# Performance work log

Hardware: AMD Instinct MI355X
Metric: run time of the kernel (lower is better)

The kernel has to match this reference:

```python
import jax, jax.numpy as jnp
import numpy as np
from jax import lax

B = 16384
D_MODEL = 84
N_EXPERTS = 2
TOP_K = 2
HIDDEN = 2048


def _conv(x, w, b):
    # x: [N,C,H,W], w: [O,I,kh,kw] (torch OIHW), VALID padding, stride 1
    y = lax.conv_general_dilated(x, w, (1, 1), 'VALID',
                                 dimension_numbers=('NCHW', 'OIHW', 'NCHW'))
    return y + b[None, :, None, None]


def _maxpool2(x):
    return lax.reduce_window(x, -jnp.inf, lax.max,
                             (1, 1, 2, 2), (1, 1, 2, 2), 'VALID')


def setup_inputs() -> dict:
    key = jax.random.key(0)
    ks = jax.random.split(key, 17)
    s = 0.05
    return {
        'x': jax.random.normal(ks[0], (B, 3, 32, 32), jnp.float32),
        'conv1_w': jax.random.normal(ks[1], (6, 3, 5, 5), jnp.float32) * s,
        'conv1_b': jax.random.normal(ks[2], (6,), jnp.float32) * s,
        'conv2_w': jax.random.normal(ks[3], (16, 6, 5, 5), jnp.float32) * s,
        'conv2_b': jax.random.normal(ks[4], (16,), jnp.float32) * s,
        'fc1_w': jax.random.normal(ks[5], (400, 120), jnp.float32) * s,
        'fc1_b': jax.random.normal(ks[6], (120,), jnp.float32) * s,
        'fc2_w': jax.random.normal(ks[7], (120, 84), jnp.float32) * s,
        'fc2_b': jax.random.normal(ks[8], (84,), jnp.float32) * s,
        'gate_w': jax.random.normal(ks[9], (D_MODEL, N_EXPERTS), jnp.float32) * s,
        'exp_w1': jax.random.normal(ks[10], (N_EXPERTS, D_MODEL, HIDDEN), jnp.float32) * s,
        'exp_b1': jax.random.normal(ks[11], (N_EXPERTS, HIDDEN), jnp.float32) * s,
        'exp_w2': jax.random.normal(ks[12], (N_EXPERTS, HIDDEN, D_MODEL), jnp.float32) * s,
        'exp_b2': jax.random.normal(ks[13], (N_EXPERTS, D_MODEL), jnp.float32) * s,
        'fc3_w': jax.random.normal(ks[14], (84, 10), jnp.float32) * s,
        'fc3_b': jax.random.normal(ks[15], (10,), jnp.float32) * s,
    }


def _moe(x, gate_w, exp_w1, exp_b1, exp_w2, exp_b2):
    # tutel top-k gate: softmax over expert logits, select top-k, renormalize
    n = x.shape[0]
    scores = jax.nn.softmax(x @ gate_w, axis=-1)          # [N,E]
    top_v, top_i = lax.top_k(scores, TOP_K)               # [N,k]
    gates = top_v / jnp.sum(top_v, axis=-1, keepdims=True)
    # dense combine weights [N,E] (zero where not routed)
    comb = jnp.zeros((n, N_EXPERTS), x.dtype).at[
        jnp.arange(n)[:, None], top_i].set(gates)
    # grouped expert FFN (E=2: evaluate both, weight-combine)
    h = jax.nn.relu(jnp.einsum('nd,edh->enh', x, exp_w1) + exp_b1[:, None, :])
    y = jnp.einsum('enh,ehd->end', h, exp_w2) + exp_b2[:, None, :]  # [E,N,D]
    return jnp.einsum('ne,end->nd', comb, y)


def reference(x, conv1_w, conv1_b, conv2_w, conv2_b, fc1_w, fc1_b,
              fc2_w, fc2_b, gate_w, exp_w1, exp_b1, exp_w2, exp_b2,
              fc3_w, fc3_b):
    h = _maxpool2(jax.nn.relu(_conv(x, conv1_w, conv1_b)))   # [B,6,14,14]
    h = _maxpool2(jax.nn.relu(_conv(h, conv2_w, conv2_b)))   # [B,16,5,5]
    h = h.reshape(-1, 16 * 5 * 5)                            # [B,400]
    h = jax.nn.relu(h @ fc1_w + fc1_b)                       # [B,120]
    h = jax.nn.relu(h @ fc2_w + fc2_b)                       # [B,84]
    h = _moe(h, gate_w, exp_w1, exp_b1, exp_w2, exp_b2)      # [B,84]
    return h @ fc3_w + fc3_b                                 # [B,10]
```

## Files before the change

### kernel.cpp

```cpp
#include <hip/hip_runtime.h>
#include <stdint.h>

typedef unsigned short u16;
typedef __attribute__((ext_vector_type(8))) short s8v;
typedef __attribute__((ext_vector_type(4))) float f4v;
typedef __fp16 h2v __attribute__((ext_vector_type(2)));

__device__ __forceinline__ float bu2f(u16 u) {
  return __uint_as_float(((uint32_t)u) << 16);
}
__device__ __forceinline__ u16 f2bu(float f) {
  uint32_t u = __float_as_uint(f);
  u += 0x7fffu + ((u >> 16) & 1u);
  return (u16)(u >> 16);
}
__device__ __forceinline__ u16 f2h16(float f) {
  __fp16 h = (__fp16)f;
  u16 r;
  __builtin_memcpy(&r, &h, 2);
  return r;
}
__device__ __forceinline__ float ldin(int m, const void* p, long i) {
  return m ? ((const float*)p)[i] : bu2f(((const u16*)p)[i]);
}

union U32H2 { uint32_t u; h2v h; };

__device__ __forceinline__ uint32_t pk2h(float a, float b) {
  U32H2 x;
  x.h = __builtin_amdgcn_cvt_pkrtz(a, b);
  return x.u;
}

#if __has_builtin(__builtin_amdgcn_fdot2)
__device__ __forceinline__ float fdot2u(uint32_t a, uint32_t b, float c) {
  U32H2 ua, ub;
  ua.u = a; ub.u = b;
  return __builtin_amdgcn_fdot2(ua.h, ub.h, c, false);
}
#else
__device__ __forceinline__ float fdot2u(uint32_t a, uint32_t b, float c) {
  U32H2 ua, ub;
  ua.u = a; ub.u = b;
  c = fmaf((float)ua.h.x, (float)ub.h.x, c);
  return fmaf((float)ua.h.y, (float)ub.h.y, c);
}
#endif

__global__ __launch_bounds__(256) void k_init(
    const u16* __restrict__ x,
    const void* __restrict__ c1w, const void* __restrict__ c1b,
    const void* __restrict__ c2w, const void* __restrict__ c2b,
    int* __restrict__ flag, uint32_t* __restrict__ cdw) {
  __shared__ int s[256];
  __shared__ int smode;
  const int tid = threadIdx.x;
  int cnt = 0;
  for (int i = tid; i < 2048; i += 256) {
    int e = (x[i] >> 7) & 0xFF;
    cnt += (e >= 96 && e <= 134) ? 1 : 0;
  }
  s[tid] = cnt;
  __syncthreads();
  if (tid == 0) {
    int t = 0;
    for (int i = 0; i < 256; ++i) t += s[i];
    int m = (t >= 1843) ? 0 : 1;
    *flag = m;
    smode = m;
  }
  __syncthreads();
  const int mode = smode;
  for (int i = tid; i < 1732; i += 256) {
    if (i < 270) {
      int p = i % 3, ky = (i / 3) % 5, ic = (i / 15) % 3, c = i / 45;
      long b = (((long)c * 3 + ic) * 5 + ky) * 5;
      float w0 = ldin(mode, c1w, b + 2 * p);
      float w1 = (2 * p + 1 < 5) ? ldin(mode, c1w, b + 2 * p + 1) : 0.f;
      cdw[i] = (uint32_t)f2h16(w0) | ((uint32_t)f2h16(w1) << 16);
    } else if (i < 1710) {
      int j = i - 270;
      int p = j % 3, ky = (j / 3) % 5, ic = (j / 15) % 6, c = j / 90;
      long b = (((long)c * 6 + ic) * 5 + ky) * 5;
      float w0 = ldin(mode, c2w, b + 2 * p);
      float w1 = (2 * p + 1 < 5) ? ldin(mode, c2w, b + 2 * p + 1) : 0.f;
      cdw[i] = (uint32_t)f2h16(w0) | ((uint32_t)f2h16(w1) << 16);
    } else if (i < 1716) {
      ((float*)(cdw + 1710))[i - 1710] = ldin(mode, c1b, i - 1710);
    } else {
      ((float*)(cdw + 1716))[i - 1716] = ldin(mode, c2b, i - 1716);
    }
  }
}

#define CIMG 5
#define SXW 38
__global__ __launch_bounds__(256, 3) void k_conv(
    const int* __restrict__ flag,
    const void* __restrict__ x,
    const uint32_t* __restrict__ cdw,
    const void* __restrict__ fc1w, const void* __restrict__ fc2w,
    const void* __restrict__ ew1, const void* __restrict__ ew2,
    u16* __restrict__ p2,
    u16* __restrict__ fc1t, u16* __restrict__ fc2t,
    u16* __restrict__ w1t, u16* __restrict__ w2t,
    int Btot) {
  __shared__ u16 sxh[CIMG * 3 * 32 * SXW];
  __shared__ u16 sp1h[CIMG * 6 * 14 * 18];
  const int mode = *flag;
  const uint32_t* cd1 = cdw;
  const uint32_t* cd2 = cdw + 270;
  const float* cb1 = (const float*)(cdw + 1710);
  const float* cb2 = (const float*)(cdw + 1716);
  const int tid = threadIdx.x;
  const long gimg0 = (long)blockIdx.x * CIMG;

  for (int r = tid; r < CIMG * 96; r += 256) {
    *(uint32_t*)(sxh + (size_t)r * SXW + 32) = 0;
    *(uint32_t*)(sxh + (size_t)r * SXW + 34) = 0;
    *(uint32_t*)(sxh + (size_t)r * SXW + 36) = 0;
  }
  for (int r = tid; r < CIMG * 84; r += 256) {
    *(uint32_t*)(sp1h + (size_t)r * 18 + 14) = 0;
    *(uint32_t*)(sp1h + (size_t)r * 18 + 16) = 0;
  }

  for (int i = tid; i < CIMG * 96; i += 256) {
    int img = i / 96, rem = i - img * 96;
    if (gimg0 + img < Btot) {
      long goff = (gimg0 + img) * 3072 + (long)rem * 32;
      u16* dst = sxh + (size_t)i * SXW;
      if (!mode) {
        const uint32_t* src = (const uint32_t*)((const u16*)x + goff);
#pragma unroll
        for (int j = 0; j < 16; ++j) {
          uint32_t d = src[j];
          *(uint32_t*)(dst + 2 * j) =
              pk2h(__uint_as_float(d << 16), __uint_as_float(d & 0xffff0000u));
        }
      } else {
        const float* src = (const float*)x + goff;
#pragma unroll
        for (int j = 0; j < 16; ++j)
          *(uint32_t*)(dst + 2 * j) = pk2h(src[2 * j], src[2 * j + 1]);
      }
    }
  }
  __syncthreads();

  for (int task = tid; task < CIMG * 196; task += 256) {
    int img = task / 196, pos = task - img * 196;
    if (gimg0 + img >= Btot) continue;
    int py = pos / 14, px = pos - py * 14;
    int x0 = 2 * px, y0 = 2 * py;
    float acc[6][4];
#pragma unroll
    for (int c = 0; c < 6; ++c) {
      float bv = cb1[c];
      acc[c][0] = bv; acc[c][1] = bv; acc[c][2] = bv; acc[c][3] = bv;
    }
    for (int ic = 0; ic < 3; ++ic) {
      uint32_t A[6][4], S[6][3];
      const u16* rb = sxh + ((size_t)(img * 3 + ic) * 32 + y0) * SXW + x0;
#pragma unroll
      for (int r = 0; r < 6; ++r) {
#pragma unroll
        for (int p = 0; p < 4; ++p)
          A[r][p] = *(const uint32_t*)(rb + (size_t)r * SXW + 2 * p);
#pragma unroll
        for (int p = 0; p < 3; ++p)
          S[r][p] = (A[r][p] >> 16) | (A[r][p + 1] << 16);
      }
#pragma unroll
      for (int c = 0; c < 6; ++c) {
        const uint32_t* wb = cd1 + ((c * 3 + ic) * 5) * 3;
#pragma unroll
        for (int ky = 0; ky < 5; ++ky) {
#pragma unroll
          for (int p = 0; p < 3; ++p) {
            uint32_t w = wb[ky * 3 + p];
            acc[c][0] = fdot2u(A[ky][p], w, acc[c][0]);
            acc[c][1] = fdot2u(S[ky][p], w, acc[c][1]);
            acc[c][2] = fdot2u(A[ky + 1][p], w, acc[c][2]);
            acc[c][3] = fdot2u(S[ky + 1][p], w, acc[c][3]);
          }
        }
      }
    }
#pragma unroll
    for (int c = 0; c < 6; ++c) {
      float m = fmaxf(0.f, fmaxf(fmaxf(acc[c][0], acc[c][1]),
                                 fmaxf(acc[c][2], acc[c][3])));
      sp1h[((size_t)(img * 6 + c) * 14 + py) * 18 + px] = f2h16(m);
    }
  }
  __syncthreads();

  for (int task = tid; task < CIMG * 100; task += 256) {
    int img = task / 100, r0 = task - img * 100;
    if (gimg0 + img >= Btot) continue;
    int grp = r0 / 25, pos = r0 - grp * 25;
    int py = pos / 5, px = pos - py * 5;
    int x0 = 2 * px, y0 = 2 * py;
    int c0 = grp * 4;
    float acc[4][4];
#pragma unroll
    for (int c = 0; c < 4; ++c) {
      float bv = cb2[c0 + c];
      acc[c][0] = bv; acc[c][1] = bv; acc[c][2] = bv; acc[c][3] = bv;
    }
    for (int ic = 0; ic < 6; ++ic) {
      uint32_t A[6][4], S[6][3];
      const u16* rb = sp1h + ((size_t)(img * 6 + ic) * 14 + y0) * 18 + x0;
#pragma unroll
      for (int r = 0; r < 6; ++r) {
#pragma unroll
        for (int p = 0; p < 4; ++p)
          A[r][p] = *(const uint32_t*)(rb + (size_t)r * 18 + 2 * p);
#pragma unroll
        for (int p = 0; p < 3; ++p)
          S[r][p] = (A[r][p] >> 16) | (A[r][p + 1] << 16);
      }
#pragma unroll
      for (int c = 0; c < 4; ++c) {
        const uint32_t* wb = cd2 + (((c0 + c) * 6 + ic) * 5) * 3;
#pragma unroll
        for (int ky = 0; ky < 5; ++ky) {
#pragma unroll
          for (int p = 0; p < 3; ++p) {
            uint32_t w = wb[ky * 3 + p];
            acc[c][0] = fdot2u(A[ky][p], w, acc[c][0]);
            acc[c][1] = fdot2u(S[ky][p], w, acc[c][1]);
            acc[c][2] = fdot2u(A[ky + 1][p], w, acc[c][2]);
            acc[c][3] = fdot2u(S[ky + 1][p], w, acc[c][3]);
          }
        }
      }
    }
    u16* pout = p2 + (gimg0 + img) * 416;
#pragma unroll
    for (int c = 0; c < 4; ++c) {
      float m = fmaxf(0.f, fmaxf(fmaxf(acc[c][0], acc[c][1]),
                                 fmaxf(acc[c][2], acc[c][3])));
      pout[(c0 + c) * 25 + py * 5 + px] = f2bu(m);
    }
  }

  for (int i = tid; i < CIMG * 16; i += 256) {
    int img = i / 16;
    if (gimg0 + img < Btot) p2[(gimg0 + img) * 416 + 400 + (i & 15)] = 0;
  }

  {
    long base = (long)blockIdx.x * 260;
    long end = base + 260;
    if (end > 851968) end = 851968;
    for (long gid = base + tid; gid < end; gid += 256) {
      if (gid < 53248) {
        int n = (int)(gid / 416), k = (int)(gid % 416);
        fc1t[gid] = (n < 120 && k < 400)
                        ? f2bu(ldin(mode, fc1w, (long)k * 120 + n)) : (u16)0;
      } else if (gid < 65536) {
        long i = gid - 53248;
        int n = (int)(i / 128), k = (int)(i % 128);
        fc2t[i] = (n < 84 && k < 120)
                      ? f2bu(ldin(mode, fc2w, (long)k * 84 + n)) : (u16)0;
      } else if (gid < 458752) {
        long i = gid - 65536;
        int e = (int)(i / 196608);
        long r = i % 196608;
        int n = (int)(r / 96), k = (int)(r % 96);
        w1t[i] = (k < 84)
                     ? f2bu(ldin(mode, ew1, ((long)e * 84 + k) * 2048 + n)) : (u16)0;
      } else {
        long i = gid - 458752;
        int e = (int)(i / 196608);
        long r = i % 196608;
        int n = (int)(r / 2048), k = (int)(r % 2048);
        w2t[i] = (n < 84)
                     ? f2bu(ldin(mode, ew2, ((long)e * 2048 + k) * 84 + n)) : (u16)0;
      }
    }
  }
}

__global__ __launch_bounds__(256, 2) void k_fcA(
    const int* __restrict__ flag,
    const u16* __restrict__ p2,
    const u16* __restrict__ fc1t, const u16* __restrict__ fc2t,
    const void* __restrict__ fc1b, const void* __restrict__ fc2b,
    const void* __restrict__ gw,
    u16* __restrict__ a2buf, float* __restrict__ scbuf) {
  __shared__ __align__(16) char smem[62976];
  u16* a2s = (u16*)smem;
  u16* hs = (u16*)(smem + 13312);
  u16* wbuf = (u16*)(smem + 31232);
  u16* xs = (u16*)(smem + 57856);

  const int mode = *flag;
  const int tid = threadIdx.x;
  const int wv = tid >> 6, ln = tid & 63;
  const int m = ln & 15, quad = ln >> 4;
  const long t0 = (long)blockIdx.x * 64;
  const int row0 = wv * 16 + quad * 4;

  for (int i = tid; i < 30720 / 4; i += 256) ((uint32_t*)smem)[i] = 0;

  f4v acc1[8];
#pragma unroll
  for (int i = 0; i < 8; ++i) acc1[i] = (f4v){0.f, 0.f, 0.f, 0.f};
  for (int s = 0; s < 13; ++s) {
    {
      int r = tid >> 2, c0 = (tid & 3) * 8;
      *(uint4*)(xs + r * 40 + c0) =
          *(const uint4*)(p2 + (t0 + r) * 416 + s * 32 + c0);
      int n = tid >> 1, cw = (tid & 1) * 16;
      *(uint4*)(wbuf + n * 40 + cw) = *(const uint4*)(fc1t + (long)n * 416 + s * 32 + cw);
      *(uint4*)(wbuf + n * 40 + cw + 8) =
          *(const uint4*)(fc1t + (long)n * 416 + s * 32 + cw + 8);
    }
    __syncthreads();
    s8v a = *(const s8v*)(xs + (wv * 16 + m) * 40 + quad * 8);
#pragma unroll
    for (int nt = 0; nt < 8; ++nt) {
      s8v b = *(const s8v*)(wbuf + (nt * 16 + m) * 40 + quad * 8);
      acc1[nt] = __builtin_amdgcn_mfma_f32_16x16x32_bf16(a, b, acc1[nt], 0, 0, 0);
    }
    __syncthreads();
  }
#pragma unroll
  for (int nt = 0; nt < 8; ++nt) {
    int n = nt * 16 + m;
    if (n < 120) {
      float bv = ldin(mode, fc1b, n);
#pragma unroll
      for (int r = 0; r < 4; ++r)
        hs[(row0 + r) * 136 + n] = f2bu(fmaxf(acc1[nt][r] + bv, 0.f));
    }
  }
  __syncthreads();

  for (int i = tid; i < 1536; i += 256) {
    int n = i >> 4, c0 = (i & 15) * 8;
    *(uint4*)(wbuf + n * 136 + c0) = *(const uint4*)(fc2t + n * 128 + c0);
  }
  __syncthreads();
  f4v acc2[6];
#pragma unroll
  for (int i = 0; i < 6; ++i) acc2[i] = (f4v){0.f, 0.f, 0.f, 0.f};
  for (int s = 0; s < 4; ++s) {
    s8v a = *(const s8v*)(hs + (wv * 16 + m) * 136 + s * 32 + quad * 8);
#pragma unroll
    for (int nt = 0; nt < 6; ++nt) {
      s8v b = *(const s8v*)(wbuf + (nt * 16 + m) * 136 + s * 32 + quad * 8);
      acc2[nt] = __builtin_amdgcn_mfma_f32_16x16x32_bf16(a, b, acc2[nt], 0, 0, 0);
    }
  }
  __syncthreads();
#pragma unroll
  for (int nt = 0; nt < 6; ++nt) {
    int n = nt * 16 + m;
    if (n < 84) {
      float bv = ldin(mode, fc2b, n);
#pragma unroll
      for (int r = 0; r < 4; ++r)
        a2s[(row0 + r) * 104 + n] = f2bu(fmaxf(acc2[nt][r] + bv, 0.f));
    }
  }
  __syncthreads();

  if (tid < 64) {
    const u16* xr = a2s + tid * 104;
    float l0 = 0.f, l1 = 0.f;
    for (int k = 0; k < 84; ++k) {
      float xv = bu2f(xr[k]);
      l0 = fmaf(xv, ldin(mode, gw, 2 * k), l0);
      l1 = fmaf(xv, ldin(mode, gw, 2 * k + 1), l1);
    }
    float mx = fmaxf(l0, l1);
    float e0 = __expf(l0 - mx), e1 = __expf(l1 - mx);
    float inv = 1.f / (e0 + e1);
    *(float2*)(scbuf + (t0 + tid) * 2) = make_float2(e0 * inv, e1 * inv);
  }
  for (int i = tid; i < 832; i += 256) {
    int r = i / 13, c0 = (i - r * 13) * 8;
    *(uint4*)(a2buf + (t0 + r) * 104 + c0) = *(const uint4*)(a2s + r * 104 + c0);
  }
}

__global__ __launch_bounds__(256, 2) void k_exp(
    const int* __restrict__ flag,
    const u16* __restrict__ a2buf, const float* __restrict__ scbuf,
    const u16* __restrict__ w1t, const u16* __restrict__ w2t,
    const void* __restrict__ eb1, const void* __restrict__ eb2,
    float* __restrict__ ybuf, int Btok) {
  __shared__ __align__(16) char smem[57856];
  u16* a2s = (u16*)smem;
  u16* hs = (u16*)(smem + 13312);
  u16* wbuf = (u16*)(smem + 30720);
  float* scs = (float*)(smem + 57344);

  const int mode = *flag;
  const int tid = threadIdx.x;
  const int wv = tid >> 6, ln = tid & 63;
  const int m = ln & 15, quad = ln >> 4;
  const int e = blockIdx.y;
  const long t0 = (long)blockIdx.x * 64;
  const int row0 = wv * 16 + quad * 4;
  const u16* w1te = w1t + (long)e * 196608;
  const u16* w2te = w2t + (long)e * 196608;

  for (int i = tid; i < 832; i += 256) {
    int r = i / 13, c0 = (i - r * 13) * 8;
    *(uint4*)(a2s + r * 104 + c0) = *(const uint4*)(a2buf + (t0 + r) * 104 + c0);
  }
  if (tid < 64) scs[tid] = scbuf[(t0 + tid) * 2 + e];
  __syncthreads();

  f4v acce[6];
#pragma unroll
  for (int i = 0; i < 6; ++i) acce[i] = (f4v){0.f, 0.f, 0.f, 0.f};
  for (int c = 0; c < 16; ++c) {
    const int n0 = c * 128;
    if (c) __syncthreads();
    for (int i = tid; i < 1536; i += 256) {
      int nl = i / 12, c0 = (i - nl * 12) * 8;
      *(uint4*)(wbuf + nl * 104 + c0) =
          *(const uint4*)(w1te + (long)(n0 + nl) * 96 + c0);
    }
    __syncthreads();
    f4v acch[8];
#pragma unroll
    for (int i = 0; i < 8; ++i) acch[i] = (f4v){0.f, 0.f, 0.f, 0.f};
    for (int s = 0; s < 3; ++s) {
      s8v a = *(const s8v*)(a2s + (wv * 16 + m) * 104 + s * 32 + quad * 8);
#pragma unroll
      for (int nt = 0; nt < 8; ++nt) {
        s8v b = *(const s8v*)(wbuf + (nt * 16 + m) * 104 + s * 32 + quad * 8);
        acch[nt] = __builtin_amdgcn_mfma_f32_16x16x32_bf16(a, b, acch[nt], 0, 0, 0);
      }
    }
#pragma unroll
    for (int nt = 0; nt < 8; ++nt) {
      float bv = ldin(mode, eb1, (long)e * 2048 + n0 + nt * 16 + m);
#pragma unroll
      for (int r = 0; r < 4; ++r)
        hs[(row0 + r) * 136 + nt * 16 + m] = f2bu(fmaxf(acch[nt][r] + bv, 0.f));
    }
    __syncthreads();
    for (int i = tid; i < 1536; i += 256) {
      int n = i >> 4, c0 = (i & 15) * 8;
      *(uint4*)(wbuf + n * 136 + c0) =
          *(const uint4*)(w2te + (long)n * 2048 + n0 + c0);
    }
    __syncthreads();
    for (int s = 0; s < 4; ++s) {
      s8v a = *(const s8v*)(hs + (wv * 16 + m) * 136 + s * 32 + quad * 8);
#pragma unroll
      for (int nt = 0; nt < 6; ++nt) {
        s8v b = *(const s8v*)(wbuf + (nt * 16 + m) * 136 + s * 32 + quad * 8);
        acce[nt] = __builtin_amdgcn_mfma_f32_16x16x32_bf16(a, b, acce[nt], 0, 0, 0);
      }
    }
  }

#pragma unroll
  for (int nt = 0; nt < 6; ++nt) {
    int d = nt * 16 + m;
    float bv = (d < 84) ? ldin(mode, eb2, (long)e * 84 + d) : 0.f;
#pragma unroll
    for (int r = 0; r < 4; ++r) {
      float sc = scs[row0 + r];
      ybuf[((size_t)e * Btok + t0 + row0 + r) * 96 + d] = sc * (acce[nt][r] + bv);
    }
  }
}

__global__ __launch_bounds__(256) void k_fc3(
    const int* __restrict__ flag,
    const float* __restrict__ ybuf,
    const void* __restrict__ w3, const void* __restrict__ b3,
    void* __restrict__ out, int Btok) {
  __shared__ float sw3[840];
  __shared__ float sb3[10];
  const int mode = *flag;
  const int tid = threadIdx.x;
  const long t0 = (long)blockIdx.x * 64;
  for (int i = tid; i < 840; i += 256) sw3[i] = ldin(mode, w3, i);
  if (tid < 10) sb3[tid] = ldin(mode, b3, tid);
  __syncthreads();
  for (int idx = tid; idx < 640; idx += 256) {
    int tk = idx / 10, cc = idx - tk * 10;
    const float* y0r = ybuf + (t0 + tk) * 96;
    const float* y1r = ybuf + ((size_t)Btok + t0 + tk) * 96;
    float acc = sb3[cc];
    for (int d = 0; d < 84; ++d)
      acc = fmaf(y0r[d] + y1r[d], sw3[d * 10 + cc], acc);
    long oi = (t0 + tk) * 10 + cc;
    if (mode) ((float*)out)[oi] = acc;
    else ((u16*)out)[oi] = f2bu(acc);
  }
}

extern "C" void kernel_launch(void* const* d_in, const int* in_sizes, int n_in,
                              void* d_out, int out_size, void* d_ws, size_t ws_size,
                              hipStream_t stream) {
  const int B = in_sizes[0] / 3072;
  char* wsb = (char*)d_ws;
  int* flag = (int*)wsb;
  u16* p2 = (u16*)(wsb + 64);
  u16* fc1t = p2 + (size_t)B * 416;
  u16* fc2t = fc1t + 53248;
  u16* w1t = fc2t + 12288;
  u16* w2t = w1t + 393216;
  uint32_t* cdw = (uint32_t*)(w2t + 393216);
  u16* a2buf = (u16*)(cdw + 1732);
  float* scbuf = (float*)(a2buf + (size_t)B * 104);
  float* ybuf = scbuf + (size_t)B * 2;

  k_init<<<1, 256, 0, stream>>>((const u16*)d_in[0], d_in[1], d_in[2],
                                d_in[3], d_in[4], flag, cdw);

  const int convGrid = (B + CIMG - 1) / CIMG;
  k_conv<<<convGrid, 256, 0, stream>>>(flag, d_in[0], cdw, d_in[5], d_in[7],
                                       d_in[10], d_in[12], p2, fc1t, fc2t,
                                       w1t, w2t, B);

  k_fcA<<<B / 64, 256, 0, stream>>>(flag, p2, fc1t, fc2t, d_in[6], d_in[8],
                                    d_in[9], a2buf, scbuf);

  dim3 eg(B / 64, 2);
  k_exp<<<eg, 256, 0, stream>>>(flag, a2buf, scbuf, w1t, w2t, d_in[11],
                                d_in[13], ybuf, B);

  k_fc3<<<B / 64, 256, 0, stream>>>(flag, ybuf, d_in[14], d_in[15], d_out, B);
}
```

Baseline: 619.0 us.

## Pre-shift conv weights, fragment-major weight layouts, direct global MFMA B loads

The conv weight tables now hold separate even- and odd-phase weight pairs, so the shifted input words no longer have to be built with shifts and ors, and the padding zero-fill is dropped. The FC and expert weight transposes are written in an MFMA-fragment-major layout, so B operands are read straight from global memory (L2-resident) instead of being staged in LDS with extra barriers. The fcA kernel stages the whole input row block in two passes and caches biases and gate weights in shared memory. The expert kernel also caches its biases in LDS and raises occupancy by using less shared memory. The trade-off is more global-load latency exposed on every MFMA B fetch and double the conv weight table size.

```diff
diff --git a/kernel.cpp b/kernel.cpp
--- a/kernel.cpp
+++ b/kernel.cpp
@@ -71,24 +71,24 @@
   }
   __syncthreads();
   const int mode = smode;
-  for (int i = tid; i < 1732; i += 256) {
-    if (i < 270) {
-      int p = i % 3, ky = (i / 3) % 5, ic = (i / 15) % 3, c = i / 45;
-      long b = (((long)c * 3 + ic) * 5 + ky) * 5;
-      float w0 = ldin(mode, c1w, b + 2 * p);
-      float w1 = (2 * p + 1 < 5) ? ldin(mode, c1w, b + 2 * p + 1) : 0.f;
+  for (int i = tid; i < 3442; i += 256) {
+    if (i < 3420) {
+      int j, icmax;
+      const void* wsrc;
+      if (i < 540) { j = i; icmax = 3; wsrc = c1w; }
+      else { j = i - 540; icmax = 6; wsrc = c2w; }
+      int p = j % 3, ph = (j / 3) % 2, ky = (j / 6) % 5;
+      int icc = (j / 30) % icmax, c = j / (30 * icmax);
+      long base = (((long)c * icmax + icc) * 5 + ky) * 5;
+      int i0 = ph ? (2 * p - 1) : (2 * p);
+      int i1 = i0 + 1;
+      float w0 = (i0 >= 0 && i0 < 5) ? ldin(mode, wsrc, base + i0) : 0.f;
+      float w1 = (i1 < 5) ? ldin(mode, wsrc, base + i1) : 0.f;
       cdw[i] = (uint32_t)f2h16(w0) | ((uint32_t)f2h16(w1) << 16);
-    } else if (i < 1710) {
-      int j = i - 270;
-      int p = j % 3, ky = (j / 3) % 5, ic = (j / 15) % 6, c = j / 90;
-      long b = (((long)c * 6 + ic) * 5 + ky) * 5;
-      float w0 = ldin(mode, c2w, b + 2 * p);
-      float w1 = (2 * p + 1 < 5) ? ldin(mode, c2w, b + 2 * p + 1) : 0.f;
-      cdw[i] = (uint32_t)f2h16(w0) | ((uint32_t)f2h16(w1) << 16);
-    } else if (i < 1716) {
-      ((float*)(cdw + 1710))[i - 1710] = ldin(mode, c1b, i - 1710);
+    } else if (i < 3426) {
+      ((float*)(cdw + 3420))[i - 3420] = ldin(mode, c1b, i - 3420);
     } else {
-      ((float*)(cdw + 1716))[i - 1716] = ldin(mode, c2b, i - 1716);
+      ((float*)(cdw + 3426))[i - 3426] = ldin(mode, c2b, i - 3426);
     }
   }
 }
@@ -109,21 +109,11 @@
   __shared__ u16 sp1h[CIMG * 6 * 14 * 18];
   const int mode = *flag;
   const uint32_t* cd1 = cdw;
-  const uint32_t* cd2 = cdw + 270;
-  const float* cb1 = (const float*)(cdw + 1710);
-  const float* cb2 = (const float*)(cdw + 1716);
+  const uint32_t* cd2 = cdw + 540;
+  const float* cb1 = (const float*)(cdw + 3420);
+  const float* cb2 = (const float*)(cdw + 3426);
   const int tid = threadIdx.x;
   const long gimg0 = (long)blockIdx.x * CIMG;
-
-  for (int r = tid; r < CIMG * 96; r += 256) {
-    *(uint32_t*)(sxh + (size_t)r * SXW + 32) = 0;
-    *(uint32_t*)(sxh + (size_t)r * SXW + 34) = 0;
-    *(uint32_t*)(sxh + (size_t)r * SXW + 36) = 0;
-  }
-  for (int r = tid; r < CIMG * 84; r += 256) {
-    *(uint32_t*)(sp1h + (size_t)r * 18 + 14) = 0;
-    *(uint32_t*)(sp1h + (size_t)r * 18 + 16) = 0;
-  }
 
   for (int i = tid; i < CIMG * 96; i += 256) {
     int img = i / 96, rem = i - img * 96;
@@ -160,29 +150,26 @@
       acc[c][0] = bv; acc[c][1] = bv; acc[c][2] = bv; acc[c][3] = bv;
     }
     for (int ic = 0; ic < 3; ++ic) {
-      uint32_t A[6][4], S[6][3];
+      uint32_t A[6][3];
       const u16* rb = sxh + ((size_t)(img * 3 + ic) * 32 + y0) * SXW + x0;
 #pragma unroll
-      for (int r = 0; r < 6; ++r) {
-#pragma unroll
-        for (int p = 0; p < 4; ++p)
+      for (int r = 0; r < 6; ++r)
+#pragma unroll
+        for (int p = 0; p < 3; ++p)
           A[r][p] = *(const uint32_t*)(rb + (size_t)r * SXW + 2 * p);
 #pragma unroll
-        for (int p = 0; p < 3; ++p)
-          S[r][p] = (A[r][p] >> 16) | (A[r][p + 1] << 16);
-      }
-#pragma unroll
       for (int c = 0; c < 6; ++c) {
-        const uint32_t* wb = cd1 + ((c * 3 + ic) * 5) * 3;
+        const uint32_t* wb = cd1 + (c * 3 + ic) * 30;
 #pragma unroll
         for (int ky = 0; ky < 5; ++ky) {
 #pragma unroll
           for (int p = 0; p < 3; ++p) {
-            uint32_t w = wb[ky * 3 + p];
-            acc[c][0] = fdot2u(A[ky][p], w, acc[c][0]);
-            acc[c][1] = fdot2u(S[ky][p], w, acc[c][1]);
-            acc[c][2] = fdot2u(A[ky + 1][p], w, acc[c][2]);
-            acc[c][3] = fdot2u(S[ky + 1][p], w, acc[c][3]);
+            uint32_t we = wb[ky * 6 + p];
+            uint32_t wo = wb[ky * 6 + 3 + p];
+            acc[c][0] = fdot2u(A[ky][p], we, acc[c][0]);
+            acc[c][1] = fdot2u(A[ky][p], wo, acc[c][1]);
+            acc[c][2] = fdot2u(A[ky + 1][p], we, acc[c][2]);
+            acc[c][3] = fdot2u(A[ky + 1][p], wo, acc[c][3]);
           }
         }
       }
@@ -210,29 +197,26 @@
       acc[c][0] = bv; acc[c][1] = bv; acc[c][2] = bv; acc[c][3] = bv;
     }
     for (int ic = 0; ic < 6; ++ic) {
-      uint32_t A[6][4], S[6][3];
+      uint32_t A[6][3];
       const u16* rb = sp1h + ((size_t)(img * 6 + ic) * 14 + y0) * 18 + x0;
 #pragma unroll
-      for (int r = 0; r < 6; ++r) {
-#pragma unroll
-        for (int p = 0; p < 4; ++p)
+      for (int r = 0; r < 6; ++r)
+#pragma unroll
+        for (int p = 0; p < 3; ++p)
           A[r][p] = *(const uint32_t*)(rb + (size_t)r * 18 + 2 * p);
 #pragma unroll
-        for (int p = 0; p < 3; ++p)
-          S[r][p] = (A[r][p] >> 16) | (A[r][p + 1] << 16);
-      }
-#pragma unroll
       for (int c = 0; c < 4; ++c) {
-        const uint32_t* wb = cd2 + (((c0 + c) * 6 + ic) * 5) * 3;
+        const uint32_t* wb = cd2 + ((c0 + c) * 6 + ic) * 30;
 #pragma unroll
         for (int ky = 0; ky < 5; ++ky) {
 #pragma unroll
           for (int p = 0; p < 3; ++p) {
-            uint32_t w = wb[ky * 3 + p];
-            acc[c][0] = fdot2u(A[ky][p], w, acc[c][0]);
-            acc[c][1] = fdot2u(S[ky][p], w, acc[c][1]);
-            acc[c][2] = fdot2u(A[ky + 1][p], w, acc[c][2]);
-            acc[c][3] = fdot2u(S[ky + 1][p], w, acc[c][3]);
+            uint32_t we = wb[ky * 6 + p];
+            uint32_t wo = wb[ky * 6 + 3 + p];
+            acc[c][0] = fdot2u(A[ky][p], we, acc[c][0]);
+            acc[c][1] = fdot2u(A[ky][p], wo, acc[c][1]);
+            acc[c][2] = fdot2u(A[ky + 1][p], we, acc[c][2]);
+            acc[c][3] = fdot2u(A[ky + 1][p], wo, acc[c][3]);
           }
         }
       }
@@ -257,26 +241,30 @@
     if (end > 851968) end = 851968;
     for (long gid = base + tid; gid < end; gid += 256) {
       if (gid < 53248) {
-        int n = (int)(gid / 416), k = (int)(gid % 416);
+        int j = (int)(gid & 7), n = (int)((gid >> 3) & 127);
+        int k = (int)((gid >> 10) * 8) + j;
         fc1t[gid] = (n < 120 && k < 400)
                         ? f2bu(ldin(mode, fc1w, (long)k * 120 + n)) : (u16)0;
       } else if (gid < 65536) {
         long i = gid - 53248;
-        int n = (int)(i / 128), k = (int)(i % 128);
+        int j = (int)(i & 7), n = (int)((i >> 3) % 96);
+        int k = (int)((i / 768) * 8) + j;
         fc2t[i] = (n < 84 && k < 120)
                       ? f2bu(ldin(mode, fc2w, (long)k * 84 + n)) : (u16)0;
       } else if (gid < 458752) {
         long i = gid - 65536;
         int e = (int)(i / 196608);
         long r = i % 196608;
-        int n = (int)(r / 96), k = (int)(r % 96);
+        int j = (int)(r & 7), n = (int)((r >> 3) & 2047);
+        int k = (int)((r >> 14) * 8) + j;
         w1t[i] = (k < 84)
                      ? f2bu(ldin(mode, ew1, ((long)e * 84 + k) * 2048 + n)) : (u16)0;
       } else {
         long i = gid - 458752;
         int e = (int)(i / 196608);
         long r = i % 196608;
-        int n = (int)(r / 2048), k = (int)(r % 2048);
+        int j = (int)(r & 7), n = (int)((r >> 3) % 96);
+        int k = (int)((r / 768) * 8) + j;
         w2t[i] = (n < 84)
                      ? f2bu(ldin(mode, ew2, ((long)e * 2048 + k) * 84 + n)) : (u16)0;
       }
@@ -284,18 +272,21 @@
   }
 }
 
-__global__ __launch_bounds__(256, 2) void k_fcA(
+#define XSW 232
+__global__ __launch_bounds__(256, 3) void k_fcA(
     const int* __restrict__ flag,
     const u16* __restrict__ p2,
     const u16* __restrict__ fc1t, const u16* __restrict__ fc2t,
     const void* __restrict__ fc1b, const void* __restrict__ fc2b,
     const void* __restrict__ gw,
     u16* __restrict__ a2buf, float* __restrict__ scbuf) {
-  __shared__ __align__(16) char smem[62976];
+  __shared__ __align__(16) char smem[48592];
+  u16* xs = (u16*)smem;
   u16* a2s = (u16*)smem;
-  u16* hs = (u16*)(smem + 13312);
-  u16* wbuf = (u16*)(smem + 31232);
-  u16* xs = (u16*)(smem + 57856);
+  u16* hs = (u16*)(smem + 29696);
+  float* sb1f = (float*)(smem + 47104);
+  float* sb2f = (float*)(smem + 47584);
+  float* sgw = (float*)(smem + 47920);
 
   const int mode = *flag;
   const int tid = threadIdx.x;
@@ -304,47 +295,53 @@
   const long t0 = (long)blockIdx.x * 64;
   const int row0 = wv * 16 + quad * 4;
 
-  for (int i = tid; i < 30720 / 4; i += 256) ((uint32_t*)smem)[i] = 0;
+  if (tid < 120) sb1f[tid] = ldin(mode, fc1b, tid);
+  if (tid < 84) sb2f[tid] = ldin(mode, fc2b, tid);
+  if (tid < 168) sgw[tid] = ldin(mode, gw, tid);
+  for (int i = tid; i < 1792; i += 256) {
+    int r = i / 28, c0 = (i - r * 28) * 8;
+    *(uint4*)(xs + r * XSW + c0) = *(const uint4*)(p2 + (t0 + r) * 416 + c0);
+  }
+  __syncthreads();
 
   f4v acc1[8];
 #pragma unroll
   for (int i = 0; i < 8; ++i) acc1[i] = (f4v){0.f, 0.f, 0.f, 0.f};
-  for (int s = 0; s < 13; ++s) {
-    {
-      int r = tid >> 2, c0 = (tid & 3) * 8;
-      *(uint4*)(xs + r * 40 + c0) =
-          *(const uint4*)(p2 + (t0 + r) * 416 + s * 32 + c0);
-      int n = tid >> 1, cw = (tid & 1) * 16;
-      *(uint4*)(wbuf + n * 40 + cw) = *(const uint4*)(fc1t + (long)n * 416 + s * 32 + cw);
-      *(uint4*)(wbuf + n * 40 + cw + 8) =
-          *(const uint4*)(fc1t + (long)n * 416 + s * 32 + cw + 8);
-    }
-    __syncthreads();
-    s8v a = *(const s8v*)(xs + (wv * 16 + m) * 40 + quad * 8);
+  for (int s = 0; s < 7; ++s) {
+    s8v a = *(const s8v*)(xs + (wv * 16 + m) * XSW + s * 32 + quad * 8);
 #pragma unroll
     for (int nt = 0; nt < 8; ++nt) {
-      s8v b = *(const s8v*)(wbuf + (nt * 16 + m) * 40 + quad * 8);
+      s8v b = *(const s8v*)(fc1t + (((long)(s * 4 + quad) * 128 + nt * 16 + m) << 3));
       acc1[nt] = __builtin_amdgcn_mfma_f32_16x16x32_bf16(a, b, acc1[nt], 0, 0, 0);
     }
-    __syncthreads();
+  }
+  __syncthreads();
+  for (int i = tid; i < 1536; i += 256) {
+    int r = i / 24, c0 = (i - r * 24) * 8;
+    *(uint4*)(xs + r * XSW + c0) =
+        *(const uint4*)(p2 + (t0 + r) * 416 + 224 + c0);
+  }
+  __syncthreads();
+  for (int s = 7; s < 13; ++s) {
+    s8v a = *(const s8v*)(xs + (wv * 16 + m) * XSW + (s - 7) * 32 + quad * 8);
+#pragma unroll
+    for (int nt = 0; nt < 8; ++nt) {
+      s8v b = *(const s8v*)(fc1t + (((long)(s * 4 + quad) * 128 + nt * 16 + m) << 3));
+      acc1[nt] = __builtin_amdgcn_mfma_f32_16x16x32_bf16(a, b, acc1[nt], 0, 0, 0);
+    }
   }
 #pragma unroll
   for (int nt = 0; nt < 8; ++nt) {
     int n = nt * 16 + m;
-    if (n < 120) {
-      float bv = ldin(mode, fc1b, n);
-#pragma unroll
-      for (int r = 0; r < 4; ++r)
-        hs[(row0 + r) * 136 + n] = f2bu(fmaxf(acc1[nt][r] + bv, 0.f));
-    }
-  }
-  __syncthreads();
-
-  for (int i = tid; i < 1536; i += 256) {
-    int n = i >> 4, c0 = (i & 15) * 8;
-    *(uint4*)(wbuf + n * 136 + c0) = *(const uint4*)(fc2t + n * 128 + c0);
-  }
-  __syncthreads();
+    float bv = (n < 120) ? sb1f[n] : 0.f;
+#pragma unroll
+    for (int r = 0; r < 4; ++r) {
+      float v = (n < 120) ? fmaxf(acc1[nt][r] + bv, 0.f) : 0.f;
+      hs[(row0 + r) * 136 + n] = f2bu(v);
+    }
+  }
+  __syncthreads();
+
   f4v acc2[6];
 #pragma unroll
   for (int i = 0; i < 6; ++i) acc2[i] = (f4v){0.f, 0.f, 0.f, 0.f};
@@ -352,19 +349,18 @@
     s8v a = *(const s8v*)(hs + (wv * 16 + m) * 136 + s * 32 + quad * 8);
 #pragma unroll
     for (int nt = 0; nt < 6; ++nt) {
-      s8v b = *(const s8v*)(wbuf + (nt * 16 + m) * 136 + s * 32 + quad * 8);
+      s8v b = *(const s8v*)(fc2t + (((long)(s * 4 + quad) * 96 + nt * 16 + m) << 3));
       acc2[nt] = __builtin_amdgcn_mfma_f32_16x16x32_bf16(a, b, acc2[nt], 0, 0, 0);
     }
   }
-  __syncthreads();
 #pragma unroll
   for (int nt = 0; nt < 6; ++nt) {
     int n = nt * 16 + m;
-    if (n < 84) {
-      float bv = ldin(mode, fc2b, n);
-#pragma unroll
-      for (int r = 0; r < 4; ++r)
-        a2s[(row0 + r) * 104 + n] = f2bu(fmaxf(acc2[nt][r] + bv, 0.f));
+    float bv = (n < 84) ? sb2f[n] : 0.f;
+#pragma unroll
+    for (int r = 0; r < 4; ++r) {
+      float v = (n < 84) ? fmaxf(acc2[nt][r] + bv, 0.f) : 0.f;
+      a2s[(row0 + r) * 104 + n] = f2bu(v);
     }
   }
   __syncthreads();
@@ -374,8 +370,8 @@
     float l0 = 0.f, l1 = 0.f;
     for (int k = 0; k < 84; ++k) {
       float xv = bu2f(xr[k]);
-      l0 = fmaf(xv, ldin(mode, gw, 2 * k), l0);
-      l1 = fmaf(xv, ldin(mode, gw, 2 * k + 1), l1);
+      l0 = fmaf(xv, sgw[2 * k], l0);
+      l1 = fmaf(xv, sgw[2 * k + 1], l1);
     }
     float mx = fmaxf(l0, l1);
     float e0 = __expf(l0 - mx), e1 = __expf(l1 - mx);
@@ -394,11 +390,12 @@
     const u16* __restrict__ w1t, const u16* __restrict__ w2t,
     const void* __restrict__ eb1, const void* __restrict__ eb2,
     float* __restrict__ ybuf, int Btok) {
-  __shared__ __align__(16) char smem[57856];
+  __shared__ __align__(16) char smem[39504];
   u16* a2s = (u16*)smem;
   u16* hs = (u16*)(smem + 13312);
-  u16* wbuf = (u16*)(smem + 30720);
-  float* scs = (float*)(smem + 57344);
+  float* sb1 = (float*)(smem + 30720);
+  float* sb2 = (float*)(smem + 38912);
+  float* scs = (float*)(smem + 39248);
 
   const int mode = *flag;
   const int tid = threadIdx.x;
@@ -414,6 +411,8 @@
     int r = i / 13, c0 = (i - r * 13) * 8;
     *(uint4*)(a2s + r * 104 + c0) = *(const uint4*)(a2buf + (t0 + r) * 104 + c0);
   }
+  for (int i = tid; i < 2048; i += 256) sb1[i] = ldin(mode, eb1, (long)e * 2048 + i);
+  if (tid < 84) sb2[tid] = ldin(mode, eb2, (long)e * 84 + tid);
   if (tid < 64) scs[tid] = scbuf[(t0 + tid) * 2 + e];
   __syncthreads();
 
@@ -422,13 +421,6 @@
   for (int i = 0; i < 6; ++i) acce[i] = (f4v){0.f, 0.f, 0.f, 0.f};
   for (int c = 0; c < 16; ++c) {
     const int n0 = c * 128;
-    if (c) __syncthreads();
-    for (int i = tid; i < 1536; i += 256) {
-      int nl = i / 12, c0 = (i - nl * 12) * 8;
-      *(uint4*)(wbuf + nl * 104 + c0) =
-          *(const uint4*)(w1te + (long)(n0 + nl) * 96 + c0);
-    }
-    __syncthreads();
     f4v acch[8];
 #pragma unroll
     for (int i = 0; i < 8; ++i) acch[i] = (f4v){0.f, 0.f, 0.f, 0.f};
@@ -436,38 +428,34 @@
       s8v a = *(const s8v*)(a2s + (wv * 16 + m) * 104 + s * 32 + quad * 8);
 #pragma unroll
       for (int nt = 0; nt < 8; ++nt) {
-        s8v b = *(const s8v*)(wbuf + (nt * 16 + m) * 104 + s * 32 + quad * 8);
+        s8v b = *(const s8v*)(w1te + (((long)(s * 4 + quad) * 2048 + n0 + nt * 16 + m) << 3));
         acch[nt] = __builtin_amdgcn_mfma_f32_16x16x32_bf16(a, b, acch[nt], 0, 0, 0);
       }
     }
 #pragma unroll
     for (int nt = 0; nt < 8; ++nt) {
-      float bv = ldin(mode, eb1, (long)e * 2048 + n0 + nt * 16 + m);
+      float bv = sb1[n0 + nt * 16 + m];
 #pragma unroll
       for (int r = 0; r < 4; ++r)
         hs[(row0 + r) * 136 + nt * 16 + m] = f2bu(fmaxf(acch[nt][r] + bv, 0.f));
     }
     __syncthreads();
-    for (int i = tid; i < 1536; i += 256) {
-      int n = i >> 4, c0 = (i & 15) * 8;
-      *(uint4*)(wbuf + n * 136 + c0) =
-          *(const uint4*)(w2te + (long)n * 2048 + n0 + c0);
-    }
-    __syncthreads();
     for (int s = 0; s < 4; ++s) {
+      int sg = c * 4 + s;
       s8v a = *(const s8v*)(hs + (wv * 16 + m) * 136 + s * 32 + quad * 8);
 #pragma unroll
       for (int nt = 0; nt < 6; ++nt) {
-        s8v b = *(const s8v*)(wbuf + (nt * 16 + m) * 136 + s * 32 + quad * 8);
+        s8v b = *(const s8v*)(w2te + (((long)(sg * 4 + quad) * 96 + nt * 16 + m) << 3));
         acce[nt] = __builtin_amdgcn_mfma_f32_16x16x32_bf16(a, b, acce[nt], 0, 0, 0);
       }
     }
+    __syncthreads();
   }
 
 #pragma unroll
   for (int nt = 0; nt < 6; ++nt) {
     int d = nt * 16 + m;
-    float bv = (d < 84) ? ldin(mode, eb2, (long)e * 84 + d) : 0.f;
+    float bv = (d < 84) ? sb2[d] : 0.f;
 #pragma unroll
     for (int r = 0; r < 4; ++r) {
       float sc = scs[row0 + r];
@@ -514,7 +502,7 @@
   u16* w1t = fc2t + 12288;
   u16* w2t = w1t + 393216;
   uint32_t* cdw = (uint32_t*)(w2t + 393216);
-  u16* a2buf = (u16*)(cdw + 1732);
+  u16* a2buf = (u16*)(cdw + 3456);
   float* scbuf = (float*)(a2buf + (size_t)B * 104);
   float* ybuf = scbuf + (size_t)B * 2;
 
```

Measured after the change: 641.4 us. 3.6% more time.
